# Kernel tuning notes

Measured on AMD Instinct MI355X. Metric: run time of the kernel, lower is better.

Reference implementation:

```python
import jax, jax.numpy as jnp
import numpy as np

N, E, D, ED = 10000, 50000, 32, 16
DIMS = [(D, 8 * D), (8 * D, 16 * D), (16 * D, 16 * D), (16 * D, 16 * D)]
BI_OUT = 8 * D + ED  # 272


def _gat(h, src, dst, ea, Wl, Wr, We, att, b, n):
    """GATv2Conv, heads=1: score = att . leaky_relu(Wl x_j + Wr x_i + We e_ij); msg = Wl x_j."""
    xl = h @ Wl
    xr = h @ Wr
    ee = ea @ We
    s = jax.nn.leaky_relu(xl[src] + xr[dst] + ee, 0.2)   # [E_aug, out]
    alpha = s @ att                                       # [E_aug]
    amax = jax.lax.stop_gradient(jax.ops.segment_max(alpha, dst, num_segments=n))
    ex = jnp.exp(alpha - amax[dst])
    den = jax.ops.segment_sum(ex, dst, num_segments=n)
    w = ex / jnp.maximum(den[dst], 1e-16)
    return jax.ops.segment_sum(xl[src] * w[:, None], dst, num_segments=n) + b


def _forward(x, edge_attr, Wl0, Wr0, We0, a0, b0, Wl1, Wr1, We1, a1, b1,
             Wl2, Wr2, We2, a2, b2, Wl3, Wr3, We3, a3, b3,
             Wbi, bbi, Wm1, bm1, Wm2, bm2, Wm3, bm3, edge_index):
    src, dst = edge_index[0], edge_index[1]
    # self loops with edge_attr fill_value='mean' (mean of incoming edge_attr per target node)
    cnt = jax.ops.segment_sum(jnp.ones((E,), jnp.float32), dst, num_segments=N)
    mean_attr = jax.ops.segment_sum(edge_attr, dst, num_segments=N) / jnp.maximum(cnt, 1.0)[:, None]
    loop = jnp.arange(N, dtype=edge_index.dtype)
    src_a = jnp.concatenate([src, loop])
    dst_a = jnp.concatenate([dst, loop])
    ea_a = jnp.concatenate([edge_attr, mean_attr], axis=0)

    h = x
    layers = [(Wl0, Wr0, We0, a0, b0), (Wl1, Wr1, We1, a1, b1),
              (Wl2, Wr2, We2, a2, b2), (Wl3, Wr3, We3, a3, b3)]
    for i, (Wl, Wr, We, a, b) in enumerate(layers):
        h = _gat(h, src_a, dst_a, ea_a, Wl, Wr, We, a, b, N)
        if i < 3:
            h = jax.nn.relu(h)

    # edge scoring: gather both endpoints, bilinear with edge_attr, then MLP -> sigmoid
    z = jnp.concatenate([h[src], h[dst]], axis=1)           # [E, 2*16*D] = [E, 1024]
    bi = jnp.einsum('ni,kij,nj->nk', z, Wbi, edge_attr) + bbi  # [E, 272]
    m = jax.nn.relu(bi @ Wm1 + bm1)
    m = jax.nn.relu(m @ Wm2 + bm2)
    return jax.nn.sigmoid(m @ Wm3 + bm3)                    # [E, 1]


def setup_inputs() -> dict:
    ki = iter(jax.random.split(jax.random.key(0), 40))

    def rn(shape, s=0.05):
        return jax.random.normal(next(ki), shape, dtype=jnp.float32) * s

    inp = {
        "x": rn((N, D), 1.0),
        "edge_attr": rn((E, ED), 1.0),
        "edge_index": jax.random.randint(next(ki), (2, E), 0, N, dtype=jnp.int32),
    }
    for i, (din, dout) in enumerate(DIMS):
        inp[f"Wl{i}"] = rn((din, dout))
        inp[f"Wr{i}"] = rn((din, dout))
        inp[f"We{i}"] = rn((ED, dout))
        inp[f"a{i}"] = rn((dout,))
        inp[f"b{i}"] = jnp.zeros((dout,), jnp.float32)
    inp["Wbi"] = rn((BI_OUT, 2 * 16 * D, ED), 0.02)
    inp["bbi"] = jnp.zeros((BI_OUT,), jnp.float32)
    inp["Wm1"] = rn((BI_OUT, BI_OUT))
    inp["bm1"] = jnp.zeros((BI_OUT,), jnp.float32)
    inp["Wm2"] = rn((BI_OUT, D))
    inp["bm2"] = jnp.zeros((D,), jnp.float32)
    inp["Wm3"] = rn((D, 1))
    inp["bm3"] = jnp.zeros((1,), jnp.float32)
    return inp


def reference(x, edge_attr, edge_index, Wl0, Wr0, We0, a0, b0, Wl1, Wr1, We1, a1, b1,
              Wl2, Wr2, We2, a2, b2, Wl3, Wr3, We3, a3, b3,
              Wbi, bbi, Wm1, bm1, Wm2, bm2, Wm3, bm3):
    return _forward(x, edge_attr, Wl0, Wr0, We0, a0, b0, Wl1, Wr1, We1, a1, b1,
                    Wl2, Wr2, We2, a2, b2, Wl3, Wr3, We3, a3, b3,
                    Wbi, bbi, Wm1, bm1, Wm2, bm2, Wm3, bm3, edge_index)
```

## Files before the change

kernel.cpp:

```cpp
#include <hip/hip_runtime.h>
#include <hip/hip_bf16.h>
#include <hip/hip_fp16.h>
#include <cstdio>

#define N_NODES 10000
#define M_NODEP 10112
#define N_EDGES 50000
#define M_EDGEP 50048
#define E_AUG   60000
#define E_AUGP  60032
#define ED      16
#define BI_OUT  272
#define KP      288

typedef __attribute__((ext_vector_type(8))) short s16x8;
typedef __attribute__((ext_vector_type(4))) short s16x4;
typedef __attribute__((ext_vector_type(8))) _Float16 h16x8;
typedef __attribute__((ext_vector_type(4))) _Float16 h16x4;
typedef __attribute__((ext_vector_type(4))) float f32x4;

__device__ inline void stc(float* p, float v){ *p = v; }
__device__ inline void stc(__hip_bfloat16* p, float v){ *p = __float2bfloat16(v); }
__device__ inline void stc(__half* p, float v){ *p = __float2half(v); }
__device__ inline float bf2f(short s){ return __uint_as_float(((unsigned)(unsigned short)s) << 16); }
__device__ inline short f2bf(float f){ __hip_bfloat16 h = __float2bfloat16(f); return *(short*)&h; }

__device__ __forceinline__ void gl2lds16(const void* g, void* l){
  __builtin_amdgcn_global_load_lds((const __attribute__((address_space(1))) void*)g,
                                   (__attribute__((address_space(3))) void*)l, 16, 0, 0);
}

__global__ void edge_attr_sum_k(const float* __restrict__ ea, const int* __restrict__ ei,
                                float* __restrict__ meanat, float* __restrict__ cntF){
  int t = blockIdx.x*256 + threadIdx.x;
  if (t >= N_EDGES*ED) return;
  int e = t >> 4, j = t & 15;
  int dst = ei[N_EDGES + e];
  atomicAdd(&meanat[dst*ED + j], ea[t]);
  if (j == 0) atomicAdd(&cntF[dst], 1.0f);
}

__global__ void mean_div_k(float* __restrict__ meanat, const float* __restrict__ cntF){
  int t = blockIdx.x*256 + threadIdx.x;
  if (t >= N_NODES*ED) return;
  meanat[t] /= fmaxf(cntF[t>>4], 1.0f);
}

__global__ void scan_k(const float* __restrict__ cntF, int* __restrict__ rowptr){
  __shared__ int s[1024];
  int tid = threadIdx.x;
  int loc[10]; int sum = 0;
  #pragma unroll
  for (int k = 0; k < 10; ++k){
    int i = tid*10 + k;
    int v = (i < N_NODES) ? ((int)cntF[i] + 1) : 0;
    loc[k] = sum; sum += v;
  }
  s[tid] = sum; __syncthreads();
  for (int off = 1; off < 1024; off <<= 1){
    int t2 = (tid >= off) ? s[tid-off] : 0;
    __syncthreads();
    s[tid] += t2;
    __syncthreads();
  }
  int pre = s[tid] - sum;
  #pragma unroll
  for (int k = 0; k < 10; ++k){
    int i = tid*10 + k;
    if (i < N_NODES) rowptr[i] = pre + loc[k];
  }
  if (tid == 1023) rowptr[N_NODES] = s[1023];
}

__global__ void scatter_k(const int* __restrict__ ei, const int* __restrict__ rowptr,
                          int* __restrict__ fill, int* __restrict__ csr){
  int e = blockIdx.x*256 + threadIdx.x;
  if (e >= E_AUG) return;
  int dst = (e < N_EDGES) ? ei[N_EDGES+e] : (e - N_EDGES);
  int pos = rowptr[dst] + atomicAdd(&fill[dst], 1);
  csr[pos] = e;
}

template<typename TC, bool BIAS, bool RELU>
__global__ __launch_bounds__(256)
void mfma_gemm_k(const __hip_bfloat16* __restrict__ A, const __hip_bfloat16* __restrict__ Bt,
                 TC* __restrict__ C, const float* __restrict__ bias,
                 int Mstore, int K, int lda, int ldb, int ldc){
  __shared__ __align__(16) __hip_bfloat16 Asm[4096];
  __shared__ __align__(16) __hip_bfloat16 Bsm[4096];
  const int tid = threadIdx.x;
  const int lane = tid & 63, wave = tid >> 6;
  const int wm = (wave >> 1) * 64, wn = (wave & 1) * 64;
  const int m0 = blockIdx.x * 128, n0 = blockIdx.y * 128;
  const int quad = lane >> 4, r16 = lane & 15;

  f32x4 acc[4][4];
  #pragma unroll
  for (int i = 0; i < 4; ++i)
    #pragma unroll
    for (int j = 0; j < 4; ++j)
      acc[i][j] = (f32x4){0.f, 0.f, 0.f, 0.f};

  const int rl = lane >> 2, cq = lane & 3;
  const int row0 = wave*32 + rl;
  const int qg = (cq - ((row0 >> 1) & 3)) & 3;
  const __hip_bfloat16* ga0 = &A[(size_t)(m0 + row0)*lda + qg*8];
  const __hip_bfloat16* ga1 = &A[(size_t)(m0 + row0 + 16)*lda + qg*8];
  const __hip_bfloat16* gb0 = &Bt[(size_t)(n0 + row0)*ldb + qg*8];
  const __hip_bfloat16* gb1 = &Bt[(size_t)(n0 + row0 + 16)*ldb + qg*8];
  __hip_bfloat16* lA0 = &Asm[(wave*32)*32];
  __hip_bfloat16* lA1 = &Asm[(wave*32 + 16)*32];
  __hip_bfloat16* lB0 = &Bsm[(wave*32)*32];
  __hip_bfloat16* lB1 = &Bsm[(wave*32 + 16)*32];

  for (int k0 = 0; k0 < K; k0 += 32){
    gl2lds16(ga0 + k0, lA0);
    gl2lds16(ga1 + k0, lA1);
    gl2lds16(gb0 + k0, lB0);
    gl2lds16(gb1 + k0, lB1);
    __syncthreads();
    s16x8 af[4], bf[4];
    #pragma unroll
    for (int i = 0; i < 4; ++i){
      int row = wm + i*16 + r16;
      af[i] = *(const s16x8*)&Asm[row*32 + (((quad + (row >> 1)) & 3) << 3)];
    }
    #pragma unroll
    for (int j = 0; j < 4; ++j){
      int row = wn + j*16 + r16;
      bf[j] = *(const s16x8*)&Bsm[row*32 + (((quad + (row >> 1)) & 3) << 3)];
    }
    #pragma unroll
    for (int i = 0; i < 4; ++i)
      #pragma unroll
      for (int j = 0; j < 4; ++j)
        acc[i][j] = __builtin_amdgcn_mfma_f32_16x16x32_bf16(af[i], bf[j], acc[i][j], 0, 0, 0);
    __syncthreads();
  }
  #pragma unroll
  for (int i = 0; i < 4; ++i){
    #pragma unroll
    for (int reg = 0; reg < 4; ++reg){
      int gr = m0 + wm + i*16 + quad*4 + reg;
      if (gr >= Mstore) continue;
      #pragma unroll
      for (int j = 0; j < 4; ++j){
        int gc = n0 + wn + j*16 + r16;
        float v = acc[i][j][reg];
        if (BIAS) v += bias[gc];
        if (RELU) v = fmaxf(v, 0.f);
        stc(&C[(size_t)gr*ldc + gc], v);
      }
    }
  }
}

__global__ void transpose_wlr_k(const float* __restrict__ Wl, const float* __restrict__ Wr,
                                __hip_bfloat16* __restrict__ WT, int din, int dn){
  int t = blockIdx.x*256 + threadIdx.x;
  if (t >= 2*din*dn) return;
  int half = t / (din*dn);
  int r = t - half*din*dn;
  int i = r / dn, j = r - i*dn;
  const float* W = half ? Wr : Wl;
  WT[(size_t)(half*dn + j)*din + i] = __float2bfloat16(W[r]);
}

__global__ void cast_h_k(const float* __restrict__ h, __hip_bfloat16* __restrict__ hb, int K){
  int t = blockIdx.x*256 + threadIdx.x;
  if (t >= M_NODEP*K) return;
  int r = t / K;
  hb[t] = (r < N_NODES) ? __float2bfloat16(h[t]) : __float2bfloat16(0.f);
}

__global__ void cast_ea_k(const float* __restrict__ ea, const float* __restrict__ meanat,
                          __hip_bfloat16* __restrict__ eab){
  int t = blockIdx.x*256 + threadIdx.x;
  if (t >= E_AUGP*32) return;
  int e = t >> 5, j = t & 31;
  float v = 0.f;
  if (j < 16){
    if (e < N_EDGES) v = ea[(size_t)e*ED + j];
    else if (e < E_AUG) v = meanat[(size_t)(e - N_EDGES)*ED + j];
  }
  eab[t] = __float2bfloat16(v);
}

__global__ void weT_k(const float* __restrict__ We, __hip_bfloat16* __restrict__ WeT, int dout){
  int t = blockIdx.x*256 + threadIdx.x;
  if (t >= dout*32) return;
  int n = t >> 5, k = t & 31;
  WeT[t] = __float2bfloat16((k < 16) ? We[(size_t)k*dout + n] : 0.f);
}

__global__ void wbi_transpose_k(const float* __restrict__ Wbi, __hip_bfloat16* __restrict__ WtAll){
  int t = blockIdx.x*256 + threadIdx.x;
  if (t >= BI_OUT*1024*ED) return;
  int k = t >> 14, r = t & 16383;
  int i = r >> 4, j = r & 15;
  int c = (k < 96) ? 0 : ((k < 192) ? 1 : 2);
  int kb = c*96;
  int base = c*3072;
  int cw = (c < 2) ? 1536 : 1280;
  int row = base + ((i >= 512) ? cw : 0) + (k - kb)*16 + j;
  WtAll[(size_t)row*512 + (i & 511)] = __float2bfloat16(Wbi[t]);
}

__global__ void prep_mlp_k(const float* __restrict__ Wm1, const float* __restrict__ bm1,
                           const float* __restrict__ Wm2, const float* __restrict__ bm2,
                           __hip_bfloat16* __restrict__ Wm1T, __hip_bfloat16* __restrict__ Wm2T,
                           float* __restrict__ bm1p, float* __restrict__ bm2p){
  int t = blockIdx.x*256 + threadIdx.x;
  if (t < 384*KP){
    int n = t / KP, k = t - n*KP;
    Wm1T[t] = __float2bfloat16((n < BI_OUT && k < BI_OUT) ? Wm1[(size_t)k*BI_OUT + n] : 0.f);
  }
  if (t < 128*KP){
    int n = t / KP, k = t - n*KP;
    Wm2T[t] = __float2bfloat16((n < 32 && k < BI_OUT) ? Wm2[(size_t)k*32 + n] : 0.f);
  }
  if (t < 384) bm1p[t] = (t < BI_OUT) ? bm1[t] : 0.f;
  if (t < 128) bm2p[t] = (t < 32) ? bm2[t] : 0.f;
}

template<int DOUT, bool RELU>
__global__ __launch_bounds__(256)
void gat_fused_k(const __hip_bfloat16* __restrict__ XLXR, const __half* __restrict__ EE,
                 const int* __restrict__ ei, const int* __restrict__ rowptr,
                 const int* __restrict__ csr, const float* __restrict__ att,
                 const float* __restrict__ b, __hip_bfloat16* __restrict__ hb){
  constexpr int NI = DOUT/64;
  constexpr int W2 = 2*DOUT;
  int wave = threadIdx.x >> 6, lane = threadIdx.x & 63;
  int n = blockIdx.x*4 + wave;
  if (n >= N_NODES) return;
  int r0 = rowptr[n], r1 = rowptr[n+1];
  int pp = r0 + lane;
  int e_l = 0, s_l = 0;
  if (pp < r1){
    e_l = csr[pp];
    s_l = (e_l < N_EDGES) ? ei[e_l] : (e_l - N_EDGES);
  }
  float xr[NI], at[NI], acc[NI];
  #pragma unroll
  for (int i = 0; i < NI; ++i){
    int d = lane*NI + i;
    xr[i]  = bf2f(((const short*)XLXR)[(size_t)n*W2 + DOUT + d]);
    at[i]  = att[d];
    acc[i] = 0.f;
  }
  float mrun = -1e30f, den = 0.f;
  for (int p = r0; p < r1; ++p){
    int idx = p - r0;
    int e, src;
    if (idx < 64){ e = __shfl(e_l, idx, 64); src = __shfl(s_l, idx, 64); }
    else { e = csr[p]; src = (e < N_EDGES) ? ei[e] : (e - N_EDGES); }
    const short* xlp = (const short*)XLXR + (size_t)src*W2 + lane*NI;
    const _Float16* eep = (const _Float16*)EE + (size_t)e*DOUT + lane*NI;
    float xl[NI];
    float a = 0.f;
    if constexpr (NI == 8){
      s16x8 xv = *(const s16x8*)xlp;
      h16x8 ev = *(const h16x8*)eep;
      #pragma unroll
      for (int i = 0; i < 8; ++i){
        xl[i] = bf2f(xv[i]);
        float v = xl[i] + xr[i] + (float)ev[i];
        v = (v > 0.f) ? v : 0.2f*v;
        a += at[i]*v;
      }
    } else {
      s16x4 xv = *(const s16x4*)xlp;
      h16x4 ev = *(const h16x4*)eep;
      #pragma unroll
      for (int i = 0; i < 4; ++i){
        xl[i] = bf2f(xv[i]);
        float v = xl[i] + xr[i] + (float)ev[i];
        v = (v > 0.f) ? v : 0.2f*v;
        a += at[i]*v;
      }
    }
    #pragma unroll
    for (int off = 32; off; off >>= 1) a += __shfl_down(a, off, 64);
    a = __shfl(a, 0, 64);
    float mnew = fmaxf(mrun, a);
    float scale = __expf(mrun - mnew);
    float w = __expf(a - mnew);
    den = den*scale + w;
    #pragma unroll
    for (int i = 0; i < NI; ++i) acc[i] = acc[i]*scale + w*xl[i];
    mrun = mnew;
  }
  float dinv = 1.0f / fmaxf(den, 1e-16f);
  if constexpr (NI == 8){
    s16x8 o;
    #pragma unroll
    for (int i = 0; i < 8; ++i){
      float v = b[lane*8 + i] + acc[i]*dinv;
      o[i] = f2bf(RELU ? fmaxf(v, 0.f) : v);
    }
    *(s16x8*)((short*)hb + (size_t)n*DOUT + lane*8) = o;
  } else {
    s16x4 o;
    #pragma unroll
    for (int i = 0; i < 4; ++i){
      float v = b[lane*4 + i] + acc[i]*dinv;
      o[i] = f2bf(RELU ? fmaxf(v, 0.f) : v);
    }
    *(s16x4*)((short*)hb + (size_t)n*DOUT + lane*4) = o;
  }
}

__global__ void bi_k(const __hip_bfloat16* __restrict__ P, const float* __restrict__ ea,
                     const int* __restrict__ ei, const float* __restrict__ bbi,
                     __hip_bfloat16* __restrict__ bi, int kb, int kcnt){
  int cw = kcnt*ED, w2 = 2*cw;
  int g = blockIdx.x*256 + threadIdx.x;
  if (g >= N_EDGES*kcnt) return;
  int n = g / kcnt, k = g - n*kcnt;
  int src = ei[n], dst = ei[N_EDGES+n];
  const __hip_bfloat16* pl = P + (size_t)src*w2 + k*ED;
  const __hip_bfloat16* pr = P + (size_t)dst*w2 + cw + k*ED;
  const float* eap = ea + (size_t)n*ED;
  float s = 0.f;
  #pragma unroll
  for (int j = 0; j < ED; ++j)
    s += eap[j]*(__bfloat162float(pl[j]) + __bfloat162float(pr[j]));
  int kg = kb + k;
  bi[(size_t)n*KP + kg] = __float2bfloat16(s + bbi[kg]);
}

__global__ void out_k(const __hip_bfloat16* __restrict__ m2, const float* __restrict__ Wm3,
                      const float* __restrict__ bm3, float* __restrict__ out){
  int n = blockIdx.x*256 + threadIdx.x;
  if (n >= N_EDGES) return;
  float acc = bm3[0];
  #pragma unroll
  for (int j = 0; j < 32; ++j) acc += __bfloat162float(m2[(size_t)n*128 + j])*Wm3[j];
  out[n] = 1.0f/(1.0f + __expf(-acc));
}

extern "C" void kernel_launch(void* const* d_in, const int* in_sizes, int n_in,
                              void* d_out, int out_size, void* d_ws, size_t ws_size,
                              hipStream_t stream) {
  const float* x   = (const float*)d_in[0];
  const float* ea  = (const float*)d_in[1];
  const int*   ei  = (const int*)d_in[2];
  const float* Wl[4]  = {(const float*)d_in[3],(const float*)d_in[8],(const float*)d_in[13],(const float*)d_in[18]};
  const float* Wr[4]  = {(const float*)d_in[4],(const float*)d_in[9],(const float*)d_in[14],(const float*)d_in[19]};
  const float* We[4]  = {(const float*)d_in[5],(const float*)d_in[10],(const float*)d_in[15],(const float*)d_in[20]};
  const float* att[4] = {(const float*)d_in[6],(const float*)d_in[11],(const float*)d_in[16],(const float*)d_in[21]};
  const float* bia[4] = {(const float*)d_in[7],(const float*)d_in[12],(const float*)d_in[17],(const float*)d_in[22]};
  const float* Wbi = (const float*)d_in[23];
  const float* bbi = (const float*)d_in[24];
  const float* Wm1 = (const float*)d_in[25];
  const float* bm1 = (const float*)d_in[26];
  const float* Wm2 = (const float*)d_in[27];
  const float* bm2 = (const float*)d_in[28];
  const float* Wm3 = (const float*)d_in[29];
  const float* bm3 = (const float*)d_in[30];
  float* out = (float*)d_out;

  char* ws = (char*)d_ws;
  size_t off = 0;
  auto alloc = [&](size_t b){ off = (off + 255) & ~(size_t)255; size_t o = off; off += b; return o; };
  size_t o_bi   = alloc((size_t)M_EDGEP*KP*2);
  size_t o_XLXR = alloc((size_t)M_NODEP*1024*2);
  size_t o_hb   = alloc((size_t)M_NODEP*512*2);
  size_t o_eab  = alloc((size_t)E_AUGP*32*2);
  size_t o_WT   = alloc((size_t)1024*512*2);
  size_t o_WtA  = alloc((size_t)8704*512*2);
  size_t o_WeT  = alloc((size_t)512*32*2);
  size_t o_EEP  = alloc((size_t)61440000);
  size_t o_Wm1T = alloc((size_t)384*KP*2);
  size_t o_Wm2T = alloc((size_t)128*KP*2);
  size_t o_bm1p = alloc(384*4);
  size_t o_bm2p = alloc(128*4);
  size_t o_ma   = alloc((size_t)N_NODES*ED*4);
  size_t o_cnt  = alloc(40000);
  size_t o_rp   = alloc(40004);
  size_t o_fill = alloc(40000);
  size_t o_csr  = alloc(240000);
  if (off > ws_size){
    fprintf(stderr, "kernel_launch: workspace too small: need %zu have %zu\n", off, ws_size);
    return;
  }

  float* meanat = (float*)(ws + o_ma);
  float* cntF   = (float*)(ws + o_cnt);
  int*   rowptr = (int*)(ws + o_rp);
  int*   fill   = (int*)(ws + o_fill);
  int*   csr    = (int*)(ws + o_csr);
  __hip_bfloat16* XLXR = (__hip_bfloat16*)(ws + o_XLXR);
  __hip_bfloat16* hb   = (__hip_bfloat16*)(ws + o_hb);
  __hip_bfloat16* eab  = (__hip_bfloat16*)(ws + o_eab);
  __hip_bfloat16* WT   = (__hip_bfloat16*)(ws + o_WT);
  __hip_bfloat16* WtA  = (__hip_bfloat16*)(ws + o_WtA);
  __hip_bfloat16* WeT  = (__hip_bfloat16*)(ws + o_WeT);
  __half*        EE    = (__half*)(ws + o_EEP);
  __hip_bfloat16* P    = (__hip_bfloat16*)(ws + o_EEP);
  __hip_bfloat16* Wm1T = (__hip_bfloat16*)(ws + o_Wm1T);
  __hip_bfloat16* Wm2T = (__hip_bfloat16*)(ws + o_Wm2T);
  float* bm1p = (float*)(ws + o_bm1p);
  float* bm2p = (float*)(ws + o_bm2p);
  __hip_bfloat16* bi = (__hip_bfloat16*)(ws + o_bi);
  __hip_bfloat16* m1 = (__hip_bfloat16*)(ws + o_EEP);
  __hip_bfloat16* m2 = (__hip_bfloat16*)(ws + o_EEP + 40000000);

  hipMemsetAsync(ws + o_ma, 0, (o_cnt - o_ma) + 40000, stream);
  hipMemsetAsync(ws + o_fill, 0, 40000, stream);
  edge_attr_sum_k<<<3125, 256, 0, stream>>>(ea, ei, meanat, cntF);
  mean_div_k<<<625, 256, 0, stream>>>(meanat, cntF);
  scan_k<<<1, 1024, 0, stream>>>(cntF, rowptr);
  scatter_k<<<235, 256, 0, stream>>>(ei, rowptr, fill, csr);

  cast_h_k<<<(M_NODEP*32 + 255)/256, 256, 0, stream>>>(x, hb, 32);
  cast_ea_k<<<(E_AUGP*32 + 255)/256, 256, 0, stream>>>(ea, meanat, eab);

  const int dins[4]  = {32, 256, 512, 512};
  const int douts[4] = {256, 512, 512, 512};
  for (int L = 0; L < 4; ++L){
    int din = dins[L], dn = douts[L];
    transpose_wlr_k<<<(2*din*dn + 255)/256, 256, 0, stream>>>(Wl[L], Wr[L], WT, din, dn);
    weT_k<<<(dn*32 + 255)/256, 256, 0, stream>>>(We[L], WeT, dn);
    dim3 g1(M_NODEP/128, 2*dn/128);
    mfma_gemm_k<__hip_bfloat16,false,false><<<g1, 256, 0, stream>>>(
        hb, WT, XLXR, nullptr, N_NODES, din, din, din, 2*dn);
    dim3 ge(E_AUGP/128, dn/128);
    mfma_gemm_k<__half,false,false><<<ge, 256, 0, stream>>>(eab, WeT, EE, nullptr, E_AUG, 32, 32, 32, dn);
    if (dn == 256)
      gat_fused_k<256,true><<<2500, 256, 0, stream>>>(XLXR, EE, ei, rowptr, csr, att[L], bia[L], hb);
    else if (L == 3)
      gat_fused_k<512,false><<<2500, 256, 0, stream>>>(XLXR, EE, ei, rowptr, csr, att[L], bia[L], hb);
    else
      gat_fused_k<512,true><<<2500, 256, 0, stream>>>(XLXR, EE, ei, rowptr, csr, att[L], bia[L], hb);
  }

  wbi_transpose_k<<<(BI_OUT*1024*ED + 255)/256, 256, 0, stream>>>(Wbi, WtA);

  const int kbs[3]   = {0, 96, 192};
  const int kcnts[3] = {96, 96, 80};
  const int bases[3] = {0, 3072, 6144};
  for (int c = 0; c < 3; ++c){
    int cw = kcnts[c]*ED, w2 = 2*cw;
    dim3 gp(M_NODEP/128, w2/128);
    mfma_gemm_k<__hip_bfloat16,false,false><<<gp, 256, 0, stream>>>(
        hb, WtA + (size_t)bases[c]*512, P, nullptr, N_NODES, 512, 512, 512, w2);
    bi_k<<<(N_EDGES*kcnts[c] + 255)/256, 256, 0, stream>>>(P, ea, ei, bbi, bi, kbs[c], kcnts[c]);
  }

  prep_mlp_k<<<(384*KP + 255)/256, 256, 0, stream>>>(Wm1, bm1, Wm2, bm2, Wm1T, Wm2T, bm1p, bm2p);
  dim3 gm1(M_EDGEP/128, 3);
  mfma_gemm_k<__hip_bfloat16,true,true><<<gm1, 256, 0, stream>>>(bi, Wm1T, m1, bm1p, M_EDGEP, KP, KP, KP, 384);
  dim3 gm2(M_EDGEP/128, 1);
  mfma_gemm_k<__hip_bfloat16,true,true><<<gm2, 256, 0, stream>>>(m1, Wm2T, m2, bm2p, M_EDGEP, KP, 384, KP, 128);
  out_k<<<(N_EDGES + 255)/256, 256, 0, stream>>>(m2, Wm3, bm3, out);
}
```

Before: 748.8 us.

## Enlarge GEMM tiles, batch weight prep into one kernel, unroll GAT edge loop by two

The MFMA GEMM block tile grows from 128x128 to 256x128, with each wave owning 64 rows across all 128 columns. Padded row counts are raised to match. All per-layer weight transposes and MLP weight prep are merged into one launch up front, which removes many small kernel launches. The GAT aggregation loop now processes two edges per iteration with xor-shuffle reductions to expose more memory-level parallelism. The cost is higher register pressure (32 accumulators per wave), fewer GEMM blocks for the small M dimensions, and a larger workspace.

```diff
diff --git a/kernel.cpp b/kernel.cpp
--- a/kernel.cpp
+++ b/kernel.cpp
@@ -4,11 +4,11 @@
 #include <cstdio>
 
 #define N_NODES 10000
-#define M_NODEP 10112
+#define M_NODEP 10240
 #define N_EDGES 50000
-#define M_EDGEP 50048
+#define M_EDGEP 50176
 #define E_AUG   60000
-#define E_AUGP  60032
+#define E_AUGP  60160
 #define ED      16
 #define BI_OUT  272
 #define KP      288
@@ -86,54 +86,58 @@
 void mfma_gemm_k(const __hip_bfloat16* __restrict__ A, const __hip_bfloat16* __restrict__ Bt,
                  TC* __restrict__ C, const float* __restrict__ bias,
                  int Mstore, int K, int lda, int ldb, int ldc){
-  __shared__ __align__(16) __hip_bfloat16 Asm[4096];
+  __shared__ __align__(16) __hip_bfloat16 Asm[8192];
   __shared__ __align__(16) __hip_bfloat16 Bsm[4096];
   const int tid = threadIdx.x;
   const int lane = tid & 63, wave = tid >> 6;
-  const int wm = (wave >> 1) * 64, wn = (wave & 1) * 64;
-  const int m0 = blockIdx.x * 128, n0 = blockIdx.y * 128;
+  const int m0 = blockIdx.x * 256, n0 = blockIdx.y * 128;
   const int quad = lane >> 4, r16 = lane & 15;
 
-  f32x4 acc[4][4];
+  f32x4 acc[4][8];
   #pragma unroll
   for (int i = 0; i < 4; ++i)
     #pragma unroll
-    for (int j = 0; j < 4; ++j)
+    for (int j = 0; j < 8; ++j)
       acc[i][j] = (f32x4){0.f, 0.f, 0.f, 0.f};
 
   const int rl = lane >> 2, cq = lane & 3;
-  const int row0 = wave*32 + rl;
-  const int qg = (cq - ((row0 >> 1) & 3)) & 3;
-  const __hip_bfloat16* ga0 = &A[(size_t)(m0 + row0)*lda + qg*8];
-  const __hip_bfloat16* ga1 = &A[(size_t)(m0 + row0 + 16)*lda + qg*8];
-  const __hip_bfloat16* gb0 = &Bt[(size_t)(n0 + row0)*ldb + qg*8];
-  const __hip_bfloat16* gb1 = &Bt[(size_t)(n0 + row0 + 16)*ldb + qg*8];
-  __hip_bfloat16* lA0 = &Asm[(wave*32)*32];
-  __hip_bfloat16* lA1 = &Asm[(wave*32 + 16)*32];
-  __hip_bfloat16* lB0 = &Bsm[(wave*32)*32];
-  __hip_bfloat16* lB1 = &Bsm[(wave*32 + 16)*32];
+  const int qg = (cq - ((rl >> 1) & 3)) & 3;
+  const __hip_bfloat16* ga[4];
+  const __hip_bfloat16* gb[2];
+  #pragma unroll
+  for (int r = 0; r < 4; ++r)
+    ga[r] = &A[(size_t)(m0 + wave*64 + r*16 + rl)*lda + qg*8];
+  #pragma unroll
+  for (int r = 0; r < 2; ++r)
+    gb[r] = &Bt[(size_t)(n0 + wave*32 + r*16 + rl)*ldb + qg*8];
+  __hip_bfloat16* lA[4];
+  __hip_bfloat16* lB[2];
+  #pragma unroll
+  for (int r = 0; r < 4; ++r) lA[r] = &Asm[(wave*64 + r*16)*32];
+  #pragma unroll
+  for (int r = 0; r < 2; ++r) lB[r] = &Bsm[(wave*32 + r*16)*32];
 
   for (int k0 = 0; k0 < K; k0 += 32){
-    gl2lds16(ga0 + k0, lA0);
-    gl2lds16(ga1 + k0, lA1);
-    gl2lds16(gb0 + k0, lB0);
-    gl2lds16(gb1 + k0, lB1);
+    #pragma unroll
+    for (int r = 0; r < 4; ++r) gl2lds16(ga[r] + k0, lA[r]);
+    #pragma unroll
+    for (int r = 0; r < 2; ++r) gl2lds16(gb[r] + k0, lB[r]);
     __syncthreads();
-    s16x8 af[4], bf[4];
+    s16x8 af[4], bf[8];
     #pragma unroll
     for (int i = 0; i < 4; ++i){
-      int row = wm + i*16 + r16;
+      int row = wave*64 + i*16 + r16;
       af[i] = *(const s16x8*)&Asm[row*32 + (((quad + (row >> 1)) & 3) << 3)];
     }
     #pragma unroll
-    for (int j = 0; j < 4; ++j){
-      int row = wn + j*16 + r16;
+    for (int j = 0; j < 8; ++j){
+      int row = j*16 + r16;
       bf[j] = *(const s16x8*)&Bsm[row*32 + (((quad + (row >> 1)) & 3) << 3)];
     }
     #pragma unroll
     for (int i = 0; i < 4; ++i)
       #pragma unroll
-      for (int j = 0; j < 4; ++j)
+      for (int j = 0; j < 8; ++j)
         acc[i][j] = __builtin_amdgcn_mfma_f32_16x16x32_bf16(af[i], bf[j], acc[i][j], 0, 0, 0);
     __syncthreads();
   }
@@ -141,11 +145,11 @@
   for (int i = 0; i < 4; ++i){
     #pragma unroll
     for (int reg = 0; reg < 4; ++reg){
-      int gr = m0 + wm + i*16 + quad*4 + reg;
+      int gr = m0 + wave*64 + i*16 + quad*4 + reg;
       if (gr >= Mstore) continue;
       #pragma unroll
-      for (int j = 0; j < 4; ++j){
-        int gc = n0 + wn + j*16 + r16;
+      for (int j = 0; j < 8; ++j){
+        int gc = n0 + j*16 + r16;
         float v = acc[i][j][reg];
         if (BIAS) v += bias[gc];
         if (RELU) v = fmaxf(v, 0.f);
@@ -155,15 +159,53 @@
   }
 }
 
-__global__ void transpose_wlr_k(const float* __restrict__ Wl, const float* __restrict__ Wr,
-                                __hip_bfloat16* __restrict__ WT, int din, int dn){
+__global__ void prep_weights_k(
+    const float* __restrict__ Wl0, const float* __restrict__ Wr0, const float* __restrict__ We0,
+    const float* __restrict__ Wl1, const float* __restrict__ Wr1, const float* __restrict__ We1,
+    const float* __restrict__ Wl2, const float* __restrict__ Wr2, const float* __restrict__ We2,
+    const float* __restrict__ Wl3, const float* __restrict__ Wr3, const float* __restrict__ We3,
+    const float* __restrict__ Wm1, const float* __restrict__ bm1,
+    const float* __restrict__ Wm2, const float* __restrict__ bm2,
+    __hip_bfloat16* __restrict__ WTa, __hip_bfloat16* __restrict__ WeTa,
+    __hip_bfloat16* __restrict__ Wm1T, __hip_bfloat16* __restrict__ Wm2T,
+    float* __restrict__ bm1p, float* __restrict__ bm2p){
   int t = blockIdx.x*256 + threadIdx.x;
-  if (t >= 2*din*dn) return;
-  int half = t / (din*dn);
-  int r = t - half*din*dn;
-  int i = r / dn, j = r - i*dn;
-  const float* W = half ? Wr : Wl;
-  WT[(size_t)(half*dn + j)*din + i] = __float2bfloat16(W[r]);
+  if (t < 16384){
+    int half = t >> 13, r = t & 8191, i = r >> 8, j = r & 255;
+    WTa[(half*256 + j)*32 + i] = __float2bfloat16(half ? Wr0[r] : Wl0[r]);
+  } else if (t < 278528){
+    int u = t - 16384, half = u >> 17, r = u & 131071, i = r >> 9, j = r & 511;
+    WTa[16384 + (half*512 + j)*256 + i] = __float2bfloat16(half ? Wr1[r] : Wl1[r]);
+  } else if (t < 802816){
+    int u = t - 278528, half = u >> 18, r = u & 262143, i = r >> 9, j = r & 511;
+    WTa[278528 + (half*512 + j)*512 + i] = __float2bfloat16(half ? Wr2[r] : Wl2[r]);
+  } else if (t < 1327104){
+    int u = t - 802816, half = u >> 18, r = u & 262143, i = r >> 9, j = r & 511;
+    WTa[802816 + (half*512 + j)*512 + i] = __float2bfloat16(half ? Wr3[r] : Wl3[r]);
+  }
+  if (t < 8192){
+    int n = t >> 5, k = t & 31;
+    WeTa[t] = __float2bfloat16((k < 16) ? We0[k*256 + n] : 0.f);
+  } else if (t < 24576){
+    int u = t - 8192, n = u >> 5, k = u & 31;
+    WeTa[t] = __float2bfloat16((k < 16) ? We1[k*512 + n] : 0.f);
+  } else if (t < 40960){
+    int u = t - 24576, n = u >> 5, k = u & 31;
+    WeTa[t] = __float2bfloat16((k < 16) ? We2[k*512 + n] : 0.f);
+  } else if (t < 57344){
+    int u = t - 40960, n = u >> 5, k = u & 31;
+    WeTa[t] = __float2bfloat16((k < 16) ? We3[k*512 + n] : 0.f);
+  }
+  if (t < 384*KP){
+    int n = t / KP, k = t - n*KP;
+    Wm1T[t] = __float2bfloat16((n < BI_OUT && k < BI_OUT) ? Wm1[(size_t)k*BI_OUT + n] : 0.f);
+  }
+  if (t < 128*KP){
+    int n = t / KP, k = t - n*KP;
+    Wm2T[t] = __float2bfloat16((n < 32 && k < BI_OUT) ? Wm2[(size_t)k*32 + n] : 0.f);
+  }
+  if (t < 384) bm1p[t] = (t < BI_OUT) ? bm1[t] : 0.f;
+  if (t < 128) bm2p[t] = (t < 32) ? bm2[t] : 0.f;
 }
 
 __global__ void cast_h_k(const float* __restrict__ h, __hip_bfloat16* __restrict__ hb, int K){
@@ -184,13 +226,6 @@
     else if (e < E_AUG) v = meanat[(size_t)(e - N_EDGES)*ED + j];
   }
   eab[t] = __float2bfloat16(v);
-}
-
-__global__ void weT_k(const float* __restrict__ We, __hip_bfloat16* __restrict__ WeT, int dout){
-  int t = blockIdx.x*256 + threadIdx.x;
-  if (t >= dout*32) return;
-  int n = t >> 5, k = t & 31;
-  WeT[t] = __float2bfloat16((k < 16) ? We[(size_t)k*dout + n] : 0.f);
 }
 
 __global__ void wbi_transpose_k(const float* __restrict__ Wbi, __hip_bfloat16* __restrict__ WtAll){
@@ -204,23 +239,6 @@
   int cw = (c < 2) ? 1536 : 1280;
   int row = base + ((i >= 512) ? cw : 0) + (k - kb)*16 + j;
   WtAll[(size_t)row*512 + (i & 511)] = __float2bfloat16(Wbi[t]);
-}
-
-__global__ void prep_mlp_k(const float* __restrict__ Wm1, const float* __restrict__ bm1,
-                           const float* __restrict__ Wm2, const float* __restrict__ bm2,
-                           __hip_bfloat16* __restrict__ Wm1T, __hip_bfloat16* __restrict__ Wm2T,
-                           float* __restrict__ bm1p, float* __restrict__ bm2p){
-  int t = blockIdx.x*256 + threadIdx.x;
-  if (t < 384*KP){
-    int n = t / KP, k = t - n*KP;
-    Wm1T[t] = __float2bfloat16((n < BI_OUT && k < BI_OUT) ? Wm1[(size_t)k*BI_OUT + n] : 0.f);
-  }
-  if (t < 128*KP){
-    int n = t / KP, k = t - n*KP;
-    Wm2T[t] = __float2bfloat16((n < 32 && k < BI_OUT) ? Wm2[(size_t)k*32 + n] : 0.f);
-  }
-  if (t < 384) bm1p[t] = (t < BI_OUT) ? bm1[t] : 0.f;
-  if (t < 128) bm2p[t] = (t < 32) ? bm2[t] : 0.f;
 }
 
 template<int DOUT, bool RELU>
@@ -250,45 +268,87 @@
     acc[i] = 0.f;
   }
   float mrun = -1e30f, den = 0.f;
-  for (int p = r0; p < r1; ++p){
-    int idx = p - r0;
-    int e, src;
-    if (idx < 64){ e = __shfl(e_l, idx, 64); src = __shfl(s_l, idx, 64); }
-    else { e = csr[p]; src = (e < N_EDGES) ? ei[e] : (e - N_EDGES); }
-    const short* xlp = (const short*)XLXR + (size_t)src*W2 + lane*NI;
-    const _Float16* eep = (const _Float16*)EE + (size_t)e*DOUT + lane*NI;
-    float xl[NI];
-    float a = 0.f;
+  int p = r0;
+  for (; p + 1 < r1; p += 2){
+    int i0 = p - r0, i1 = i0 + 1;
+    int e0, s0, e1, s1;
+    if (i1 < 64){
+      e0 = __shfl(e_l, i0, 64); s0 = __shfl(s_l, i0, 64);
+      e1 = __shfl(e_l, i1, 64); s1 = __shfl(s_l, i1, 64);
+    } else {
+      if (i0 < 64){ e0 = __shfl(e_l, i0, 64); s0 = __shfl(s_l, i0, 64); }
+      else { e0 = csr[p]; s0 = (e0 < N_EDGES) ? ei[e0] : (e0 - N_EDGES); }
+      e1 = csr[p+1]; s1 = (e1 < N_EDGES) ? ei[e1] : (e1 - N_EDGES);
+    }
+    const short* xp0 = (const short*)XLXR + (size_t)s0*W2 + lane*NI;
+    const short* xp1 = (const short*)XLXR + (size_t)s1*W2 + lane*NI;
+    const _Float16* ep0 = (const _Float16*)EE + (size_t)e0*DOUT + lane*NI;
+    const _Float16* ep1 = (const _Float16*)EE + (size_t)e1*DOUT + lane*NI;
+    float xl0[NI], xl1[NI];
+    float a0 = 0.f, a1 = 0.f;
     if constexpr (NI == 8){
-      s16x8 xv = *(const s16x8*)xlp;
-      h16x8 ev = *(const h16x8*)eep;
+      s16x8 xv0 = *(const s16x8*)xp0; h16x8 ev0 = *(const h16x8*)ep0;
+      s16x8 xv1 = *(const s16x8*)xp1; h16x8 ev1 = *(const h16x8*)ep1;
       #pragma unroll
       for (int i = 0; i < 8; ++i){
-        xl[i] = bf2f(xv[i]);
-        float v = xl[i] + xr[i] + (float)ev[i];
-        v = (v > 0.f) ? v : 0.2f*v;
-        a += at[i]*v;
+        xl0[i] = bf2f(xv0[i]); xl1[i] = bf2f(xv1[i]);
+        float v0 = xl0[i] + xr[i] + (float)ev0[i];
+        float v1 = xl1[i] + xr[i] + (float)ev1[i];
+        v0 = (v0 > 0.f) ? v0 : 0.2f*v0;
+        v1 = (v1 > 0.f) ? v1 : 0.2f*v1;
+        a0 += at[i]*v0; a1 += at[i]*v1;
       }
     } else {
-      s16x4 xv = *(const s16x4*)xlp;
-      h16x4 ev = *(const h16x4*)eep;
+      s16x4 xv0 = *(const s16x4*)xp0; h16x4 ev0 = *(const h16x4*)ep0;
+      s16x4 xv1 = *(const s16x4*)xp1; h16x4 ev1 = *(const h16x4*)ep1;
       #pragma unroll
       for (int i = 0; i < 4; ++i){
-        xl[i] = bf2f(xv[i]);
-        float v = xl[i] + xr[i] + (float)ev[i];
-        v = (v > 0.f) ? v : 0.2f*v;
-        a += at[i]*v;
+        xl0[i] = bf2f(xv0[i]); xl1[i] = bf2f(xv1[i]);
+        float v0 = xl0[i] + xr[i] + (float)ev0[i];
+        float v1 = xl1[i] + xr[i] + (float)ev1[i];
+        v0 = (v0 > 0.f) ? v0 : 0.2f*v0;
+        v1 = (v1 > 0.f) ? v1 : 0.2f*v1;
+        a0 += at[i]*v0; a1 += at[i]*v1;
       }
     }
     #pragma unroll
-    for (int off = 32; off; off >>= 1) a += __shfl_down(a, off, 64);
-    a = __shfl(a, 0, 64);
-    float mnew = fmaxf(mrun, a);
-    float scale = __expf(mrun - mnew);
-    float w = __expf(a - mnew);
-    den = den*scale + w;
-    #pragma unroll
-    for (int i = 0; i < NI; ++i) acc[i] = acc[i]*scale + w*xl[i];
+    for (int off = 32; off; off >>= 1){
+      a0 += __shfl_xor(a0, off, 64);
+      a1 += __shfl_xor(a1, off, 64);
+    }
+    float mnew = fmaxf(mrun, fmaxf(a0, a1));
+    float s = __expf(mrun - mnew);
+    float w0 = __expf(a0 - mnew);
+    float w1 = __expf(a1 - mnew);
+    den = den*s + w0 + w1;
+    #pragma unroll
+    for (int i = 0; i < NI; ++i) acc[i] = acc[i]*s + w0*xl0[i] + w1*xl1[i];
+    mrun = mnew;
+  }
+  if (p < r1){
+    int i0 = p - r0;
+    int e0, s0;
+    if (i0 < 64){ e0 = __shfl(e_l, i0, 64); s0 = __shfl(s_l, i0, 64); }
+    else { e0 = csr[p]; s0 = (e0 < N_EDGES) ? ei[e0] : (e0 - N_EDGES); }
+    const short* xp0 = (const short*)XLXR + (size_t)s0*W2 + lane*NI;
+    const _Float16* ep0 = (const _Float16*)EE + (size_t)e0*DOUT + lane*NI;
+    float xl0[NI];
+    float a0 = 0.f;
+    #pragma unroll
+    for (int i = 0; i < NI; ++i){
+      xl0[i] = bf2f(xp0[i]);
+      float v0 = xl0[i] + xr[i] + (float)ep0[i];
+      v0 = (v0 > 0.f) ? v0 : 0.2f*v0;
+      a0 += at[i]*v0;
+    }
+    #pragma unroll
+    for (int off = 32; off; off >>= 1) a0 += __shfl_xor(a0, off, 64);
+    float mnew = fmaxf(mrun, a0);
+    float s = __expf(mrun - mnew);
+    float w0 = __expf(a0 - mnew);
+    den = den*s + w0;
+    #pragma unroll
+    for (int i = 0; i < NI; ++i) acc[i] = acc[i]*s + w0*xl0[i];
     mrun = mnew;
   }
   float dinv = 1.0f / fmaxf(den, 1e-16f);
@@ -368,10 +428,10 @@
   size_t o_XLXR = alloc((size_t)M_NODEP*1024*2);
   size_t o_hb   = alloc((size_t)M_NODEP*512*2);
   size_t o_eab  = alloc((size_t)E_AUGP*32*2);
-  size_t o_WT   = alloc((size_t)1024*512*2);
+  size_t o_WTa  = alloc((size_t)1327104*2);
+  size_t o_WeTa = alloc((size_t)57344*2);
   size_t o_WtA  = alloc((size_t)8704*512*2);
-  size_t o_WeT  = alloc((size_t)512*32*2);
-  size_t o_EEP  = alloc((size_t)61440000);
+  size_t o_EEP  = alloc((size_t)63000000);
   size_t o_Wm1T = alloc((size_t)384*KP*2);
   size_t o_Wm2T = alloc((size_t)128*KP*2);
   size_t o_bm1p = alloc(384*4);
@@ -394,9 +454,9 @@
   __hip_bfloat16* XLXR = (__hip_bfloat16*)(ws + o_XLXR);
   __hip_bfloat16* hb   = (__hip_bfloat16*)(ws + o_hb);
   __hip_bfloat16* eab  = (__hip_bfloat16*)(ws + o_eab);
-  __hip_bfloat16* WT   = (__hip_bfloat16*)(ws + o_WT);
+  __hip_bfloat16* WTa  = (__hip_bfloat16*)(ws + o_WTa);
+  __hip_bfloat16* WeTa = (__hip_bfloat16*)(ws + o_WeTa);
   __hip_bfloat16* WtA  = (__hip_bfloat16*)(ws + o_WtA);
-  __hip_bfloat16* WeT  = (__hip_bfloat16*)(ws + o_WeT);
   __half*        EE    = (__half*)(ws + o_EEP);
   __hip_bfloat16* P    = (__hip_bfloat16*)(ws + o_EEP);
   __hip_bfloat16* Wm1T = (__hip_bfloat16*)(ws + o_Wm1T);
@@ -416,18 +476,23 @@
 
   cast_h_k<<<(M_NODEP*32 + 255)/256, 256, 0, stream>>>(x, hb, 32);
   cast_ea_k<<<(E_AUGP*32 + 255)/256, 256, 0, stream>>>(ea, meanat, eab);
+  prep_weights_k<<<5184, 256, 0, stream>>>(
+      Wl[0], Wr[0], We[0], Wl[1], Wr[1], We[1], Wl[2], Wr[2], We[2], Wl[3], Wr[3], We[3],
+      Wm1, bm1, Wm2, bm2, WTa, WeTa, Wm1T, Wm2T, bm1p, bm2p);
+  wbi_transpose_k<<<(BI_OUT*1024*ED + 255)/256, 256, 0, stream>>>(Wbi, WtA);
 
   const int dins[4]  = {32, 256, 512, 512};
   const int douts[4] = {256, 512, 512, 512};
+  const int wtOff[4] = {0, 16384, 278528, 802816};
+  const int weOff[4] = {0, 8192, 24576, 40960};
   for (int L = 0; L < 4; ++L){
     int din = dins[L], dn = douts[L];
-    transpose_wlr_k<<<(2*din*dn + 255)/256, 256, 0, stream>>>(Wl[L], Wr[L], WT, din, dn);
-    weT_k<<<(dn*32 + 255)/256, 256, 0, stream>>>(We[L], WeT, dn);
-    dim3 g1(M_NODEP/128, 2*dn/128);
+    dim3 g1(M_NODEP/256, 2*dn/128);
     mfma_gemm_k<__hip_bfloat16,false,false><<<g1, 256, 0, stream>>>(
-        hb, WT, XLXR, nullptr, N_NODES, din, din, din, 2*dn);
-    dim3 ge(E_AUGP/128, dn/128);
-    mfma_gemm_k<__half,false,false><<<ge, 256, 0, stream>>>(eab, WeT, EE, nullptr, E_AUG, 32, 32, 32, dn);
+        hb, WTa + wtOff[L], XLXR, nullptr, N_NODES, din, din, din, 2*dn);
+    dim3 ge(E_AUGP/256, dn/128);
+    mfma_gemm_k<__half,false,false><<<ge, 256, 0, stream>>>(
+        eab, WeTa + weOff[L], EE, nullptr, E_AUG, 32, 32, 32, dn);
     if (dn == 256)
       gat_fused_k<256,true><<<2500, 256, 0, stream>>>(XLXR, EE, ei, rowptr, csr, att[L], bia[L], hb);
     else if (L == 3)
@@ -436,23 +501,20 @@
       gat_fused_k<512,true><<<2500, 256, 0, stream>>>(XLXR, EE, ei, rowptr, csr, att[L], bia[L], hb);
   }
 
-  wbi_transpose_k<<<(BI_OUT*1024*ED + 255)/256, 256, 0, stream>>>(Wbi, WtA);
-
   const int kbs[3]   = {0, 96, 192};
   const int kcnts[3] = {96, 96, 80};
   const int bases[3] = {0, 3072, 6144};
   for (int c = 0; c < 3; ++c){
     int cw = kcnts[c]*ED, w2 = 2*cw;
-    dim3 gp(M_NODEP/128, w2/128);
+    dim3 gp(M_NODEP/256, w2/128);
     mfma_gemm_k<__hip_bfloat16,false,false><<<gp, 256, 0, stream>>>(
         hb, WtA + (size_t)bases[c]*512, P, nullptr, N_NODES, 512, 512, 512, w2);
     bi_k<<<(N_EDGES*kcnts[c] + 255)/256, 256, 0, stream>>>(P, ea, ei, bbi, bi, kbs[c], kcnts[c]);
   }
 
-  prep_mlp_k<<<(384*KP + 255)/256, 256, 0, stream>>>(Wm1, bm1, Wm2, bm2, Wm1T, Wm2T, bm1p, bm2p);
-  dim3 gm1(M_EDGEP/128, 3);
+  dim3 gm1(M_EDGEP/256, 3);
   mfma_gemm_k<__hip_bfloat16,true,true><<<gm1, 256, 0, stream>>>(bi, Wm1T, m1, bm1p, M_EDGEP, KP, KP, KP, 384);
-  dim3 gm2(M_EDGEP/128, 1);
+  dim3 gm2(M_EDGEP/256, 1);
   mfma_gemm_k<__hip_bfloat16,true,true><<<gm2, 256, 0, stream>>>(m1, Wm2T, m2, bm2p, M_EDGEP, KP, 384, KP, 128);
   out_k<<<(N_EDGES + 255)/256, 256, 0, stream>>>(m2, Wm3, bm3, out);
 }
```

New measurement: 893.8 us. 1.19x slower.
